# Kernel optimization log

Measured on AMD Instinct MI355X. Metric: run time of the kernel, lower is better.

Reference implementation:

```python
import jax, jax.numpy as jnp
import numpy as np

BATCH = 8192
IN_F = 1024
OUT_F = 1024
GRID_SIZE = 5
SPLINE_ORDER = 3
GRID_LO, GRID_HI = -1.0, 1.0


def setup_inputs() -> dict:
    key = jax.random.key(0)
    k1, k2, k3, k4 = jax.random.split(key, 4)
    x = jax.random.normal(k1, (BATCH, IN_F), dtype=jnp.float32)
    # grid buffer: extended knot vector, same for every input feature
    h = (GRID_HI - GRID_LO) / GRID_SIZE
    knots = jnp.linspace(GRID_LO - SPLINE_ORDER * h, GRID_HI + SPLINE_ORDER * h,
                         GRID_SIZE + 2 * SPLINE_ORDER + 1, dtype=jnp.float32)
    grid = jnp.tile(knots[None, :], (IN_F, 1))  # [in, 12]
    fan_in_scale = 1.0 / np.sqrt(IN_F)
    base_weight = jax.random.normal(k2, (OUT_F, IN_F), dtype=jnp.float32) * fan_in_scale
    spline_weight = jax.random.normal(k3, (IN_F, GRID_SIZE + SPLINE_ORDER, OUT_F), dtype=jnp.float32) * 0.1
    spline_scaler = jax.random.normal(k4, (IN_F, OUT_F), dtype=jnp.float32) * fan_in_scale
    return {"x": x, "grid": grid, "base_weight": base_weight,
            "spline_weight": spline_weight, "spline_scaler": spline_scaler}


def b_splines(x, grid):
    """Cox-de Boor recursion. x: [B, in], grid: [in, G+2k+1] -> [B, in, G+k]."""
    xe = x[:, :, None]  # [B, in, 1]
    bases = ((xe >= grid[:, :-1]) & (xe < grid[:, 1:])).astype(x.dtype)  # [B, in, G+2k]
    for k in range(1, SPLINE_ORDER + 1):
        left = (xe - grid[:, :-(k + 1)]) / (grid[:, k:-1] - grid[:, :-(k + 1)])
        right = (grid[:, k + 1:] - xe) / (grid[:, k + 1:] - grid[:, 1:-k])
        bases = left * bases[:, :, :-1] + right * bases[:, :, 1:]
    return bases  # [B, in, G+k]


def reference(x, grid, base_weight, spline_weight, spline_scaler):
    # base branch: SiLU(x) @ W_base^T
    base_out = jax.nn.silu(x) @ base_weight.T  # [B, out]
    # spline branch
    basis = b_splines(x, grid)  # [B, in, G+k]
    scaled_w = spline_weight * spline_scaler[:, None, :]  # [in, G+k, out]
    spline_out = jnp.einsum('bik,iko->bo', basis, scaled_w)  # [B, out]
    return base_out + spline_out
```

## Files before the change

kernel.cpp:

```cpp
#include <hip/hip_runtime.h>
#include <cstdint>
#include <cstddef>

#define BATCH 8192
#define IN_F 1024
#define OUT_F 1024
#define NSPL 9
#define KDIM (IN_F * NSPL)

#define BM 256
#define BN 256
#define KS (KDIM / 2)
#define NH (KS / 32)

typedef __bf16 bf16x8 __attribute__((ext_vector_type(8)));
typedef float f32x4 __attribute__((ext_vector_type(4)));

__device__ __forceinline__ void g2l16(const void* g, void* l) {
  __builtin_amdgcn_global_load_lds(
      (__attribute__((address_space(1))) void*)(g),
      (__attribute__((address_space(3))) void*)(l),
      16, 0, 0);
}

__device__ __forceinline__ void barrier_raw() {
  asm volatile("" ::: "memory");
  __builtin_amdgcn_s_barrier();
  asm volatile("" ::: "memory");
}

__global__ void build_w(const float* __restrict__ bw, const float* __restrict__ sw,
                        const float* __restrict__ sc, __bf16* __restrict__ Wt) {
  __shared__ float s_sw[16 * 8 * 64];
  __shared__ float s_sc[16 * 64];
  __shared__ float s_bw[64 * 16];
  const int tid = threadIdx.x;
  const int o0 = (blockIdx.x & 15) * 64;
  const int i0 = (blockIdx.x >> 4) * 16;

#pragma unroll
  for (int it = 0; it < 32; ++it) {
    const int t = it * 256 + tid;
    const int i = t >> 9, r = (t >> 6) & 7, oo = t & 63;
    s_sw[t] = sw[((size_t)(i0 + i) * 8 + r) * OUT_F + o0 + oo];
  }
#pragma unroll
  for (int it = 0; it < 4; ++it) {
    const int t = it * 256 + tid;
    const int i = t >> 6, oo = t & 63;
    s_sc[t] = sc[(size_t)(i0 + i) * OUT_F + o0 + oo];
  }
#pragma unroll
  for (int it = 0; it < 4; ++it) {
    const int t = it * 256 + tid;
    const int oo = t >> 4, ii = t & 15;
    s_bw[t] = bw[(size_t)(o0 + oo) * IN_F + i0 + ii];
  }
  __syncthreads();

  const int oo = tid >> 2;
  const int isub = (tid & 3) * 4;
#pragma unroll
  for (int is = 0; is < 4; ++is) {
    const int i = isub + is;
    __bf16* dst = Wt + (size_t)(o0 + oo) * KDIM + (size_t)(i0 + i) * NSPL;
    dst[0] = (__bf16)s_bw[oo * 16 + i];
    const float scal = s_sc[i * 64 + oo];
#pragma unroll
    for (int r = 0; r < 8; ++r)
      dst[1 + r] = (__bf16)(s_sw[i * 512 + r * 64 + oo] * scal);
  }
}

__global__ __launch_bounds__(256) void build_a(const float* __restrict__ x,
                                               __bf16* __restrict__ A) {
  __shared__ __align__(16) __bf16 rowbuf[2 * KDIM];
  const int tid = threadIdx.x;
  const int r2 = tid >> 7;
  const int tr = tid & 127;
  const size_t b = (size_t)blockIdx.x * 2 + r2;

  const float4* xp = (const float4*)(x + b * IN_F + (size_t)tr * 8);
  const float4 v0 = xp[0], v1 = xp[1];
  const float vv[8] = {v0.x, v0.y, v0.z, v0.w, v1.x, v1.y, v1.z, v1.w};

  union HB { __bf16 h[72]; uint4 q[9]; } hb;

#pragma unroll
  for (int f = 0; f < 8; ++f) {
    const float v = vv[f];
    const float s0 = v / (1.f + __expf(-v));
    const float p = (v + 2.2f) * 2.5f;
    const int cell = (int)floorf(p);
    const bool ok = (cell >= 0) && (cell <= 10) && (v < 2.2f);
    const float gate = ok ? (1.f / 6.f) : 0.f;
    const float t = p - (float)cell;
    const float t2 = t * t, t3 = t2 * t;
    const float omt = 1.f - t;
    const float c0 = gate * omt * omt * omt;
    const float c1 = gate * (3.f * t3 - 6.f * t2 + 4.f);
    const float c2 = gate * (-3.f * t3 + 3.f * t2 + 3.f * t + 1.f);
    const float c3 = gate * t3;
    const int j0 = cell - 3;
    hb.h[f * 9 + 0] = (__bf16)s0;
#pragma unroll
    for (int r = 0; r < 8; ++r) {
      const int d = r - j0;
      float val = (d == 0) ? c0 : 0.f;
      val = (d == 1) ? c1 : val;
      val = (d == 2) ? c2 : val;
      val = (d == 3) ? c3 : val;
      hb.h[f * 9 + 1 + r] = (__bf16)val;
    }
  }

  uint4* ldst = (uint4*)(rowbuf + (size_t)r2 * KDIM) + (size_t)tr * 9;
#pragma unroll
  for (int k = 0; k < 9; ++k) ldst[k] = hb.q[k];
  __syncthreads();

  const uint4* src = (const uint4*)rowbuf;
  uint4* dst = (uint4*)(A + (size_t)blockIdx.x * 2 * KDIM);
#pragma unroll
  for (int it = 0; it < 9; ++it)
    dst[it * 256 + tid] = src[it * 256 + tid];
}

__global__ __launch_bounds__(512, 2) void gemm_bt(const __bf16* __restrict__ A,
                                                  const __bf16* __restrict__ W,
                                                  float* __restrict__ out,
                                                  float* __restrict__ part) {
  __shared__ __align__(16) __bf16 As[4][BM * 32];
  __shared__ __align__(16) __bf16 Bs[4][BN * 32];

  const int tid = threadIdx.x;
  const int wv = tid >> 6;
  const int lane = tid & 63;

  const int bid = blockIdx.x;
  const int xcd = bid & 7;
  const int j = bid >> 3;
  const int m0 = (xcd * 4 + (j & 3)) * BM;
  const int n0 = ((j >> 2) & 3) * BN;
  const int ks = j >> 4;
  const size_t kbase = (size_t)ks * KS;

  const int wr = wv >> 2;
  const int wc = wv & 3;

  const int srow = lane >> 2;
  const int usrc = (lane & 3) ^ ((lane >> 3) & 3);
  const __bf16* gA = A + (size_t)(m0 + wv * 32 + srow) * KDIM + kbase + usrc * 8;
  const __bf16* gB = W + (size_t)(n0 + wv * 32 + srow) * KDIM + kbase + usrc * 8;

#define STAGE_HALF(s, hh)                                             \
  do {                                                                \
    const size_t ko = (size_t)(hh) * 32;                              \
    g2l16(gA + ko,                     &As[s][wv * 1024]);            \
    g2l16(gA + ko + 16 * (size_t)KDIM, &As[s][wv * 1024 + 512]);      \
    g2l16(gB + ko,                     &Bs[s][wv * 1024]);            \
    g2l16(gB + ko + 16 * (size_t)KDIM, &Bs[s][wv * 1024 + 512]);      \
  } while (0)

  const int mrow = lane & 15;
  const int quad = lane >> 4;
  const int xu = (quad ^ ((mrow >> 1) & 3)) * 8;
  int aoff[8], boff[4];
#pragma unroll
  for (int mt = 0; mt < 8; ++mt) aoff[mt] = (wr * 128 + mt * 16 + mrow) * 32 + xu;
#pragma unroll
  for (int nt = 0; nt < 4; ++nt) boff[nt] = (wc * 64 + nt * 16 + mrow) * 32 + xu;

  f32x4 acc[8][4];
  const f32x4 zero = {0.f, 0.f, 0.f, 0.f};
#pragma unroll
  for (int mt = 0; mt < 8; ++mt)
#pragma unroll
    for (int nt = 0; nt < 4; ++nt) acc[mt][nt] = zero;

  STAGE_HALF(0, 0);
  STAGE_HALF(1, 1);
  STAGE_HALF(2, 2);
  asm volatile("s_waitcnt vmcnt(8)" ::: "memory");
  barrier_raw();

  for (int h = 0; h < NH; ++h) {
    const int s = h & 3;

    bf16x8 af[8], bf[4];
#pragma unroll
    for (int mt = 0; mt < 8; ++mt) af[mt] = *(const bf16x8*)(&As[s][aoff[mt]]);
#pragma unroll
    for (int nt = 0; nt < 4; ++nt) bf[nt] = *(const bf16x8*)(&Bs[s][boff[nt]]);

    if (h + 3 < NH) {
      STAGE_HALF((h + 3) & 3, h + 3);
      asm volatile("s_waitcnt vmcnt(8)" ::: "memory");
    } else if (h + 2 < NH) {
      asm volatile("s_waitcnt vmcnt(4)" ::: "memory");
    } else {
      asm volatile("s_waitcnt vmcnt(0)" ::: "memory");
    }
    barrier_raw();

    __builtin_amdgcn_s_setprio(1);
#pragma unroll
    for (int mt = 0; mt < 8; ++mt)
#pragma unroll
      for (int nt = 0; nt < 4; ++nt)
        acc[mt][nt] = __builtin_amdgcn_mfma_f32_16x16x32_bf16(af[mt], bf[nt],
                                                              acc[mt][nt], 0, 0, 0);
    __builtin_amdgcn_s_setprio(0);
    barrier_raw();
  }

  float* __restrict__ dst = ks ? part : out;
#pragma unroll
  for (int mt = 0; mt < 8; ++mt) {
#pragma unroll
    for (int nt = 0; nt < 4; ++nt) {
      const int col = n0 + wc * 64 + nt * 16 + mrow;
      const int rbase = m0 + wr * 128 + mt * 16 + quad * 4;
#pragma unroll
      for (int r = 0; r < 4; ++r)
        dst[(size_t)(rbase + r) * OUT_F + col] = acc[mt][nt][r];
    }
  }
#undef STAGE_HALF
}

__global__ __launch_bounds__(256) void reduce_add(float* __restrict__ out,
                                                  const float* __restrict__ part) {
  const size_t base = (size_t)blockIdx.x * 256 + threadIdx.x;
  f32x4* o = (f32x4*)out;
  const f32x4* p = (const f32x4*)part;
#pragma unroll
  for (int it = 0; it < 4; ++it) {
    const size_t i = base + (size_t)it * 2048 * 256;
    f32x4 a = o[i], b = p[i];
    a.x += b.x; a.y += b.y; a.z += b.z; a.w += b.w;
    o[i] = a;
  }
}

extern "C" void kernel_launch(void* const* d_in, const int* in_sizes, int n_in,
                              void* d_out, int out_size, void* d_ws, size_t ws_size,
                              hipStream_t stream) {
  const float* x  = (const float*)d_in[0];
  const float* bw = (const float*)d_in[2];
  const float* sw = (const float*)d_in[3];
  const float* sc = (const float*)d_in[4];
  float* out = (float*)d_out;

  __bf16* Wt = (__bf16*)d_ws;
  __bf16* Ab = (__bf16*)((char*)d_ws +
                         (size_t)OUT_F * KDIM * sizeof(__bf16));
  float* part = (float*)((char*)d_ws +
                         (size_t)OUT_F * KDIM * sizeof(__bf16) +
                         (size_t)BATCH * KDIM * sizeof(__bf16));

  build_w<<<1024, 256, 0, stream>>>(bw, sw, sc, Wt);
  build_a<<<BATCH / 2, 256, 0, stream>>>(x, Ab);
  gemm_bt<<<(BATCH / BM) * (OUT_F / BN) * 2, 512, 0, stream>>>(Ab, Wt, out, part);
  reduce_add<<<2048, 256, 0, stream>>>(out, part);
}
```

Measured before the change: 291.2 us.

## Stage build_w output through LDS and split GEMM MFMA loop into two phases

build_w now writes its bf16 tile into shared memory and then stores it to global memory as coalesced 8-byte chunks, replacing the scattered 2-byte stores. In the GEMM main loop, A fragments are loaded from LDS in two halves, with extra barriers between two MFMA phases. The split is meant to interleave LDS reads with matrix ops across waves and reduce register pressure. It adds two barriers per K iteration, and the stage holding those A rows must stay valid until the second read.

```diff
diff --git a/kernel.cpp b/kernel.cpp
--- a/kernel.cpp
+++ b/kernel.cpp
@@ -29,11 +29,14 @@
   asm volatile("" ::: "memory");
 }
 
-__global__ void build_w(const float* __restrict__ bw, const float* __restrict__ sw,
-                        const float* __restrict__ sc, __bf16* __restrict__ Wt) {
+__global__ __launch_bounds__(256) void build_w(const float* __restrict__ bw,
+                                               const float* __restrict__ sw,
+                                               const float* __restrict__ sc,
+                                               __bf16* __restrict__ Wt) {
   __shared__ float s_sw[16 * 8 * 64];
   __shared__ float s_sc[16 * 64];
   __shared__ float s_bw[64 * 16];
+  __shared__ __align__(16) __bf16 s_out[64 * 144];
   const int tid = threadIdx.x;
   const int o0 = (blockIdx.x & 15) * 64;
   const int i0 = (blockIdx.x >> 4) * 16;
@@ -63,12 +66,22 @@
 #pragma unroll
   for (int is = 0; is < 4; ++is) {
     const int i = isub + is;
-    __bf16* dst = Wt + (size_t)(o0 + oo) * KDIM + (size_t)(i0 + i) * NSPL;
+    __bf16* dst = s_out + oo * 144 + i * 9;
     dst[0] = (__bf16)s_bw[oo * 16 + i];
     const float scal = s_sc[i * 64 + oo];
 #pragma unroll
     for (int r = 0; r < 8; ++r)
       dst[1 + r] = (__bf16)(s_sw[i * 512 + r * 64 + oo] * scal);
+  }
+  __syncthreads();
+
+  const uint2* s2 = (const uint2*)s_out;
+#pragma unroll
+  for (int k = 0; k < 9; ++k) {
+    const int idx = k * 256 + tid;
+    const int row = idx / 36;
+    const int col = idx - row * 36;
+    *(uint2*)(Wt + (size_t)(o0 + row) * KDIM + (size_t)i0 * 9 + col * 4) = s2[idx];
   }
 }
 
@@ -187,9 +200,9 @@
   for (int h = 0; h < NH; ++h) {
     const int s = h & 3;
 
-    bf16x8 af[8], bf[4];
-#pragma unroll
-    for (int mt = 0; mt < 8; ++mt) af[mt] = *(const bf16x8*)(&As[s][aoff[mt]]);
+    bf16x8 af[4], bf[4];
+#pragma unroll
+    for (int mt = 0; mt < 4; ++mt) af[mt] = *(const bf16x8*)(&As[s][aoff[mt]]);
 #pragma unroll
     for (int nt = 0; nt < 4; ++nt) bf[nt] = *(const bf16x8*)(&Bs[s][boff[nt]]);
 
@@ -205,11 +218,27 @@
 
     __builtin_amdgcn_s_setprio(1);
 #pragma unroll
-    for (int mt = 0; mt < 8; ++mt)
+    for (int mt = 0; mt < 4; ++mt)
 #pragma unroll
       for (int nt = 0; nt < 4; ++nt)
         acc[mt][nt] = __builtin_amdgcn_mfma_f32_16x16x32_bf16(af[mt], bf[nt],
                                                               acc[mt][nt], 0, 0, 0);
+    __builtin_amdgcn_s_setprio(0);
+    barrier_raw();
+
+    bf16x8 af2[4];
+#pragma unroll
+    for (int mt = 0; mt < 4; ++mt) af2[mt] = *(const bf16x8*)(&As[s][aoff[4 + mt]]);
+    barrier_raw();
+
+    __builtin_amdgcn_s_setprio(1);
+#pragma unroll
+    for (int mt = 0; mt < 4; ++mt)
+#pragma unroll
+      for (int nt = 0; nt < 4; ++nt)
+        acc[4 + mt][nt] = __builtin_amdgcn_mfma_f32_16x16x32_bf16(af2[mt], bf[nt],
+                                                                  acc[4 + mt][nt],
+                                                                  0, 0, 0);
     __builtin_amdgcn_s_setprio(0);
     barrier_raw();
   }
```

Measured after the change: 307.4 us. 5.6% more time.

## Compute spline basis on the fly inside GEMM instead of materializing A

Applied to the files above, without the earlier changes.

Stops writing the full expanded bf16 activation matrix (batch x 9216) to global memory. Instead the GEMM computes the B-spline bases from a transposed fp32 copy of x while staging LDS tiles; only the SiLU part is precomputed and loaded asynchronously. The weight matrix is re-laid out so that the base columns come first and the 8 spline columns per feature follow contiguously. This removes large global writes and reads for A, at the cost of extra VALU work and LDS stores inside the GEMM's main loop, which may compete with the MFMA work.

```diff
diff --git a/kernel.cpp b/kernel.cpp
--- a/kernel.cpp
+++ b/kernel.cpp
@@ -5,13 +5,12 @@
 #define BATCH 8192
 #define IN_F 1024
 #define OUT_F 1024
-#define NSPL 9
-#define KDIM (IN_F * NSPL)
+#define KDIM 9216
+#define KS 4608
+#define NH 144
 
 #define BM 256
 #define BN 256
-#define KS (KDIM / 2)
-#define NH (KS / 32)
 
 typedef __bf16 bf16x8 __attribute__((ext_vector_type(8)));
 typedef float f32x4 __attribute__((ext_vector_type(4)));
@@ -29,11 +28,38 @@
   asm volatile("" ::: "memory");
 }
 
-__global__ void build_w(const float* __restrict__ bw, const float* __restrict__ sw,
-                        const float* __restrict__ sc, __bf16* __restrict__ Wt) {
+__device__ __forceinline__ uint4 spline8(float v) {
+  const float p = (v + 2.2f) * 2.5f;
+  const int cell = (int)floorf(p);
+  const bool ok = (cell >= 0) && (cell <= 10) && (v < 2.2f);
+  const float gate = ok ? (1.f / 6.f) : 0.f;
+  const float t = p - (float)cell;
+  const float t2 = t * t, t3 = t2 * t;
+  const float omt = 1.f - t;
+  const float c0 = gate * omt * omt * omt;
+  const float c1 = gate * (3.f * t3 - 6.f * t2 + 4.f);
+  const float c2 = gate * (-3.f * t3 + 3.f * t2 + 3.f * t + 1.f);
+  const float c3 = gate * t3;
+  const int j0 = cell - 3;
+  union { __bf16 h[8]; uint4 q; } u;
+#pragma unroll
+  for (int r = 0; r < 8; ++r) {
+    const int d = r - j0;
+    float val = (d == 0) ? c0 : 0.f;
+    val = (d == 1) ? c1 : val;
+    val = (d == 2) ? c2 : val;
+    val = (d == 3) ? c3 : val;
+    u.h[r] = (__bf16)val;
+  }
+  return u.q;
+}
+
+__global__ __launch_bounds__(256) void build_w(const float* __restrict__ bw,
+                                               const float* __restrict__ sw,
+                                               const float* __restrict__ sc,
+                                               __bf16* __restrict__ Wt) {
   __shared__ float s_sw[16 * 8 * 64];
   __shared__ float s_sc[16 * 64];
-  __shared__ float s_bw[64 * 16];
   const int tid = threadIdx.x;
   const int o0 = (blockIdx.x & 15) * 64;
   const int i0 = (blockIdx.x >> 4) * 16;
@@ -50,12 +76,6 @@
     const int i = t >> 6, oo = t & 63;
     s_sc[t] = sc[(size_t)(i0 + i) * OUT_F + o0 + oo];
   }
-#pragma unroll
-  for (int it = 0; it < 4; ++it) {
-    const int t = it * 256 + tid;
-    const int oo = t >> 4, ii = t & 15;
-    s_bw[t] = bw[(size_t)(o0 + oo) * IN_F + i0 + ii];
-  }
   __syncthreads();
 
   const int oo = tid >> 2;
@@ -63,71 +83,55 @@
 #pragma unroll
   for (int is = 0; is < 4; ++is) {
     const int i = isub + is;
-    __bf16* dst = Wt + (size_t)(o0 + oo) * KDIM + (size_t)(i0 + i) * NSPL;
-    dst[0] = (__bf16)s_bw[oo * 16 + i];
     const float scal = s_sc[i * 64 + oo];
+    union { __bf16 h[8]; uint4 q; } u;
 #pragma unroll
     for (int r = 0; r < 8; ++r)
-      dst[1 + r] = (__bf16)(s_sw[i * 512 + r * 64 + oo] * scal);
-  }
-}
-
-__global__ __launch_bounds__(256) void build_a(const float* __restrict__ x,
-                                               __bf16* __restrict__ A) {
-  __shared__ __align__(16) __bf16 rowbuf[2 * KDIM];
+      u.h[r] = (__bf16)(s_sw[i * 512 + r * 64 + oo] * scal);
+    *(uint4*)(Wt + (size_t)(o0 + oo) * KDIM + 1024 + (size_t)(i0 + i) * 8) = u.q;
+  }
+
+  if ((blockIdx.x >> 4) == 0) {
+#pragma unroll
+    for (int it = 0; it < 64; ++it) {
+      const int idx = it * 256 + tid;
+      const int ooo = idx >> 8, c4 = idx & 255;
+      const float4 v = *(const float4*)(bw + (size_t)(o0 + ooo) * IN_F + c4 * 4);
+      union { __bf16 h[4]; uint2 u2; } u;
+      u.h[0] = (__bf16)v.x; u.h[1] = (__bf16)v.y;
+      u.h[2] = (__bf16)v.z; u.h[3] = (__bf16)v.w;
+      *(uint2*)(Wt + (size_t)(o0 + ooo) * KDIM + c4 * 4) = u.u2;
+    }
+  }
+}
+
+__global__ __launch_bounds__(256) void build_prep(const float* __restrict__ x,
+                                                  float* __restrict__ xT,
+                                                  __bf16* __restrict__ Asl) {
+  __shared__ float tile[64 * 65];
   const int tid = threadIdx.x;
-  const int r2 = tid >> 7;
-  const int tr = tid & 127;
-  const size_t b = (size_t)blockIdx.x * 2 + r2;
-
-  const float4* xp = (const float4*)(x + b * IN_F + (size_t)tr * 8);
-  const float4 v0 = xp[0], v1 = xp[1];
-  const float vv[8] = {v0.x, v0.y, v0.z, v0.w, v1.x, v1.y, v1.z, v1.w};
-
-  union HB { __bf16 h[72]; uint4 q[9]; } hb;
-
-#pragma unroll
-  for (int f = 0; f < 8; ++f) {
-    const float v = vv[f];
-    const float s0 = v / (1.f + __expf(-v));
-    const float p = (v + 2.2f) * 2.5f;
-    const int cell = (int)floorf(p);
-    const bool ok = (cell >= 0) && (cell <= 10) && (v < 2.2f);
-    const float gate = ok ? (1.f / 6.f) : 0.f;
-    const float t = p - (float)cell;
-    const float t2 = t * t, t3 = t2 * t;
-    const float omt = 1.f - t;
-    const float c0 = gate * omt * omt * omt;
-    const float c1 = gate * (3.f * t3 - 6.f * t2 + 4.f);
-    const float c2 = gate * (-3.f * t3 + 3.f * t2 + 3.f * t + 1.f);
-    const float c3 = gate * t3;
-    const int j0 = cell - 3;
-    hb.h[f * 9 + 0] = (__bf16)s0;
-#pragma unroll
-    for (int r = 0; r < 8; ++r) {
-      const int d = r - j0;
-      float val = (d == 0) ? c0 : 0.f;
-      val = (d == 1) ? c1 : val;
-      val = (d == 2) ? c2 : val;
-      val = (d == 3) ? c3 : val;
-      hb.h[f * 9 + 1 + r] = (__bf16)val;
-    }
-  }
-
-  uint4* ldst = (uint4*)(rowbuf + (size_t)r2 * KDIM) + (size_t)tr * 9;
-#pragma unroll
-  for (int k = 0; k < 9; ++k) ldst[k] = hb.q[k];
+  const int b0 = (blockIdx.x >> 4) * 64;
+  const int c0 = (blockIdx.x & 15) * 64;
+#pragma unroll
+  for (int it = 0; it < 16; ++it) {
+    const int idx = it * 256 + tid;
+    const int r = idx >> 6, c = idx & 63;
+    const float v = x[(size_t)(b0 + r) * IN_F + c0 + c];
+    tile[r * 65 + c] = v;
+    Asl[(size_t)(b0 + r) * IN_F + c0 + c] = (__bf16)(v / (1.f + __expf(-v)));
+  }
   __syncthreads();
-
-  const uint4* src = (const uint4*)rowbuf;
-  uint4* dst = (uint4*)(A + (size_t)blockIdx.x * 2 * KDIM);
-#pragma unroll
-  for (int it = 0; it < 9; ++it)
-    dst[it * 256 + tid] = src[it * 256 + tid];
-}
-
-__global__ __launch_bounds__(512, 2) void gemm_bt(const __bf16* __restrict__ A,
+#pragma unroll
+  for (int it = 0; it < 16; ++it) {
+    const int idx = it * 256 + tid;
+    const int f = idx >> 6, rr = idx & 63;
+    xT[(size_t)(c0 + f) * BATCH + b0 + rr] = tile[rr * 65 + f];
+  }
+}
+
+__global__ __launch_bounds__(512, 2) void gemm_bt(const __bf16* __restrict__ Asl,
                                                   const __bf16* __restrict__ W,
+                                                  const float* __restrict__ xT,
                                                   float* __restrict__ out,
                                                   float* __restrict__ part) {
   __shared__ __align__(16) __bf16 As[4][BM * 32];
@@ -150,17 +154,13 @@
 
   const int srow = lane >> 2;
   const int usrc = (lane & 3) ^ ((lane >> 3) & 3);
-  const __bf16* gA = A + (size_t)(m0 + wv * 32 + srow) * KDIM + kbase + usrc * 8;
-  const __bf16* gB = W + (size_t)(n0 + wv * 32 + srow) * KDIM + kbase + usrc * 8;
-
-#define STAGE_HALF(s, hh)                                             \
-  do {                                                                \
-    const size_t ko = (size_t)(hh) * 32;                              \
-    g2l16(gA + ko,                     &As[s][wv * 1024]);            \
-    g2l16(gA + ko + 16 * (size_t)KDIM, &As[s][wv * 1024 + 512]);      \
-    g2l16(gB + ko,                     &Bs[s][wv * 1024]);            \
-    g2l16(gB + ko + 16 * (size_t)KDIM, &Bs[s][wv * 1024 + 512]);      \
-  } while (0)
+  const __bf16* gB  = W   + (size_t)(n0 + wv * 32 + srow) * KDIM + kbase + usrc * 8;
+  const __bf16* gAs = Asl + (size_t)(m0 + wv * 32 + srow) * IN_F + usrc * 8;
+
+  const int arow_c = tid & 255;
+  const int ajc = tid >> 8;
+  const int u0x = (2 * ajc) ^ ((arow_c >> 1) & 3);
+  const int u1x = (2 * ajc + 1) ^ ((arow_c >> 1) & 3);
 
   const int mrow = lane & 15;
   const int quad = lane >> 4;
@@ -171,6 +171,30 @@
 #pragma unroll
   for (int nt = 0; nt < 4; ++nt) boff[nt] = (wc * 64 + nt * 16 + mrow) * 32 + xu;
 
+#define ISSUE(s3, t3, XN)                                                     \
+  do {                                                                        \
+    if (ks == 0 && (t3) < 32) {                                               \
+      g2l16(gAs + (size_t)(t3) * 32,              &As[s3][wv * 1024]);        \
+      g2l16(gAs + (size_t)(t3) * 32 + 16 * IN_F,  &As[s3][wv * 1024 + 512]);  \
+    } else {                                                                  \
+      const int i0_ = ks ? (448 + 4 * (t3)) : (4 * (t3) - 128);               \
+      XN.x = xT[(size_t)(i0_ + 2 * ajc) * BATCH + m0 + arow_c];               \
+      XN.y = xT[(size_t)(i0_ + 2 * ajc + 1) * BATCH + m0 + arow_c];           \
+    }                                                                         \
+    g2l16(gB + (size_t)(t3) * 32,                     &Bs[s3][wv * 1024]);    \
+    g2l16(gB + (size_t)(t3) * 32 + 16 * (size_t)KDIM, &Bs[s3][wv * 1024 + 512]); \
+  } while (0)
+
+#define COMPUTE(s2, t2, XC)                                                   \
+  do {                                                                        \
+    if (ks || (t2) >= 32) {                                                   \
+      const uint4 q0 = spline8(XC.x);                                         \
+      const uint4 q1 = spline8(XC.y);                                         \
+      *(uint4*)(&As[s2][arow_c * 32 + u0x * 8]) = q0;                         \
+      *(uint4*)(&As[s2][arow_c * 32 + u1x * 8]) = q1;                         \
+    }                                                                         \
+  } while (0)
+
   f32x4 acc[8][4];
   const f32x4 zero = {0.f, 0.f, 0.f, 0.f};
 #pragma unroll
@@ -178,40 +202,49 @@
 #pragma unroll
     for (int nt = 0; nt < 4; ++nt) acc[mt][nt] = zero;
 
-  STAGE_HALF(0, 0);
-  STAGE_HALF(1, 1);
-  STAGE_HALF(2, 2);
+  float2 xp0 = {0.f, 0.f}, xp1 = {0.f, 0.f}, xa = {0.f, 0.f}, xb = {0.f, 0.f};
+  ISSUE(0, 0, xp0);
+  ISSUE(1, 1, xp1);
+  ISSUE(2, 2, xa);
   asm volatile("s_waitcnt vmcnt(8)" ::: "memory");
+  COMPUTE(0, 0, xp0);
+  asm volatile("s_waitcnt vmcnt(4)" ::: "memory");
+  COMPUTE(1, 1, xp1);
+  asm volatile("s_waitcnt lgkmcnt(0)" ::: "memory");
   barrier_raw();
 
-  for (int h = 0; h < NH; ++h) {
-    const int s = h & 3;
-
-    bf16x8 af[8], bf[4];
-#pragma unroll
-    for (int mt = 0; mt < 8; ++mt) af[mt] = *(const bf16x8*)(&As[s][aoff[mt]]);
-#pragma unroll
-    for (int nt = 0; nt < 4; ++nt) bf[nt] = *(const bf16x8*)(&Bs[s][boff[nt]]);
-
-    if (h + 3 < NH) {
-      STAGE_HALF((h + 3) & 3, h + 3);
-      asm volatile("s_waitcnt vmcnt(8)" ::: "memory");
-    } else if (h + 2 < NH) {
-      asm volatile("s_waitcnt vmcnt(4)" ::: "memory");
-    } else {
-      asm volatile("s_waitcnt vmcnt(0)" ::: "memory");
-    }
-    barrier_raw();
-
-    __builtin_amdgcn_s_setprio(1);
-#pragma unroll
-    for (int mt = 0; mt < 8; ++mt)
-#pragma unroll
-      for (int nt = 0; nt < 4; ++nt)
-        acc[mt][nt] = __builtin_amdgcn_mfma_f32_16x16x32_bf16(af[mt], bf[nt],
-                                                              acc[mt][nt], 0, 0, 0);
-    __builtin_amdgcn_s_setprio(0);
-    barrier_raw();
+#define PHASE(h, XC, XN)                                                      \
+  do {                                                                        \
+    const int s_ = (h) & 3;                                                   \
+    bf16x8 af[8], bf[4];                                                      \
+    _Pragma("unroll")                                                         \
+    for (int mt = 0; mt < 8; ++mt) af[mt] = *(const bf16x8*)(&As[s_][aoff[mt]]); \
+    _Pragma("unroll")                                                         \
+    for (int nt = 0; nt < 4; ++nt) bf[nt] = *(const bf16x8*)(&Bs[s_][boff[nt]]); \
+    if ((h) + 3 < NH) { ISSUE(((h) + 3) & 3, (h) + 3, XN); }                  \
+    if ((h) + 2 < NH) {                                                       \
+      if ((h) + 3 < NH) { asm volatile("s_waitcnt vmcnt(4)" ::: "memory"); }  \
+      else              { asm volatile("s_waitcnt vmcnt(0)" ::: "memory"); }  \
+      COMPUTE(((h) + 2) & 3, (h) + 2, XC);                                    \
+    } else if ((h) + 1 < NH) {                                                \
+      asm volatile("s_waitcnt vmcnt(0)" ::: "memory");                        \
+    }                                                                         \
+    asm volatile("s_waitcnt lgkmcnt(0)" ::: "memory");                        \
+    barrier_raw();                                                            \
+    __builtin_amdgcn_s_setprio(1);                                            \
+    _Pragma("unroll")                                                         \
+    for (int mt = 0; mt < 8; ++mt)                                            \
+      _Pragma("unroll")                                                       \
+      for (int nt = 0; nt < 4; ++nt)                                          \
+        acc[mt][nt] = __builtin_amdgcn_mfma_f32_16x16x32_bf16(af[mt], bf[nt], \
+                                                              acc[mt][nt], 0, 0, 0); \
+    __builtin_amdgcn_s_setprio(0);                                            \
+    barrier_raw();                                                            \
+  } while (0)
+
+  for (int h = 0; h < NH; h += 2) {
+    PHASE(h, xa, xb);
+    PHASE(h + 1, xb, xa);
   }
 
   float* __restrict__ dst = ks ? part : out;
@@ -226,7 +259,9 @@
         dst[(size_t)(rbase + r) * OUT_F + col] = acc[mt][nt][r];
     }
   }
-#undef STAGE_HALF
+#undef PHASE
+#undef COMPUTE
+#undef ISSUE
 }
 
 __global__ __launch_bounds__(256) void reduce_add(float* __restrict__ out,
@@ -252,15 +287,17 @@
   const float* sc = (const float*)d_in[4];
   float* out = (float*)d_out;
 
-  __bf16* Wt = (__bf16*)d_ws;
-  __bf16* Ab = (__bf16*)((char*)d_ws +
-                         (size_t)OUT_F * KDIM * sizeof(__bf16));
-  float* part = (float*)((char*)d_ws +
-                         (size_t)OUT_F * KDIM * sizeof(__bf16) +
-                         (size_t)BATCH * KDIM * sizeof(__bf16));
+  char* ws = (char*)d_ws;
+  __bf16* Wt  = (__bf16*)ws;
+  __bf16* Asl = (__bf16*)(ws + (size_t)OUT_F * KDIM * 2);
+  float*  xT  = (float*)(ws + (size_t)OUT_F * KDIM * 2
+                            + (size_t)BATCH * IN_F * 2);
+  float* part = (float*)(ws + (size_t)OUT_F * KDIM * 2
+                            + (size_t)BATCH * IN_F * 2
+                            + (size_t)IN_F * BATCH * 4);
 
   build_w<<<1024, 256, 0, stream>>>(bw, sw, sc, Wt);
-  build_a<<<BATCH / 2, 256, 0, stream>>>(x, Ab);
-  gemm_bt<<<(BATCH / BM) * (OUT_F / BN) * 2, 512, 0, stream>>>(Ab, Wt, out, part);
+  build_prep<<<2048, 256, 0, stream>>>(x, xT, Asl);
+  gemm_bt<<<256, 512, 0, stream>>>(Asl, Wt, xT, out, part);
   reduce_add<<<2048, 256, 0, stream>>>(out, part);
 }
```

Result: slower. 399.3 us (+37.1%).

## Shrink GEMM tile to 256x128 with 4 waves and triple buffering; stage build_w output in LDS

Applied to the files above, without the earlier changes.

The GEMM block tile drops from 256x256 with 8 waves to 256x128 with 4 waves. Each wave still computes a 128x64 subtile. The LDS pipeline goes from a 4-stage ring to a 3-stage ring with a prefetch distance of two. The grid doubles so more blocks fit on each CU, at the cost of lower operand reuse per block and more total A traffic. Separately, build_w now assembles each output tile in shared memory and writes it back with coalesced 8-byte stores instead of scattered 2-byte stores.

```diff
diff --git a/kernel.cpp b/kernel.cpp
--- a/kernel.cpp
+++ b/kernel.cpp
@@ -9,7 +9,7 @@
 #define KDIM (IN_F * NSPL)
 
 #define BM 256
-#define BN 256
+#define BN 128
 #define KS (KDIM / 2)
 #define NH (KS / 32)
 
@@ -29,11 +29,14 @@
   asm volatile("" ::: "memory");
 }
 
-__global__ void build_w(const float* __restrict__ bw, const float* __restrict__ sw,
-                        const float* __restrict__ sc, __bf16* __restrict__ Wt) {
+__global__ __launch_bounds__(256) void build_w(const float* __restrict__ bw,
+                                               const float* __restrict__ sw,
+                                               const float* __restrict__ sc,
+                                               __bf16* __restrict__ Wt) {
   __shared__ float s_sw[16 * 8 * 64];
   __shared__ float s_sc[16 * 64];
   __shared__ float s_bw[64 * 16];
+  __shared__ __align__(16) __bf16 s_out[64 * 144];
   const int tid = threadIdx.x;
   const int o0 = (blockIdx.x & 15) * 64;
   const int i0 = (blockIdx.x >> 4) * 16;
@@ -63,12 +66,22 @@
 #pragma unroll
   for (int is = 0; is < 4; ++is) {
     const int i = isub + is;
-    __bf16* dst = Wt + (size_t)(o0 + oo) * KDIM + (size_t)(i0 + i) * NSPL;
+    __bf16* dst = s_out + oo * 144 + i * 9;
     dst[0] = (__bf16)s_bw[oo * 16 + i];
     const float scal = s_sc[i * 64 + oo];
 #pragma unroll
     for (int r = 0; r < 8; ++r)
       dst[1 + r] = (__bf16)(s_sw[i * 512 + r * 64 + oo] * scal);
+  }
+  __syncthreads();
+
+  const uint2* s2 = (const uint2*)s_out;
+#pragma unroll
+  for (int k = 0; k < 9; ++k) {
+    const int idx = k * 256 + tid;
+    const int row = idx / 36;
+    const int col = idx - row * 36;
+    *(uint2*)(Wt + (size_t)(o0 + row) * KDIM + (size_t)i0 * 9 + col * 4) = s2[idx];
   }
 }
 
@@ -126,12 +139,12 @@
     dst[it * 256 + tid] = src[it * 256 + tid];
 }
 
-__global__ __launch_bounds__(512, 2) void gemm_bt(const __bf16* __restrict__ A,
+__global__ __launch_bounds__(256, 2) void gemm_bt(const __bf16* __restrict__ A,
                                                   const __bf16* __restrict__ W,
                                                   float* __restrict__ out,
                                                   float* __restrict__ part) {
-  __shared__ __align__(16) __bf16 As[4][BM * 32];
-  __shared__ __align__(16) __bf16 Bs[4][BN * 32];
+  __shared__ __align__(16) __bf16 As[3][BM * 32];
+  __shared__ __align__(16) __bf16 Bs[3][BN * 32];
 
   const int tid = threadIdx.x;
   const int wv = tid >> 6;
@@ -141,25 +154,27 @@
   const int xcd = bid & 7;
   const int j = bid >> 3;
   const int m0 = (xcd * 4 + (j & 3)) * BM;
-  const int n0 = ((j >> 2) & 3) * BN;
-  const int ks = j >> 4;
+  const int n0 = ((j >> 2) & 7) * BN;
+  const int ks = j >> 5;
   const size_t kbase = (size_t)ks * KS;
 
-  const int wr = wv >> 2;
-  const int wc = wv & 3;
+  const int wr = wv >> 1;
+  const int wc = wv & 1;
 
   const int srow = lane >> 2;
   const int usrc = (lane & 3) ^ ((lane >> 3) & 3);
-  const __bf16* gA = A + (size_t)(m0 + wv * 32 + srow) * KDIM + kbase + usrc * 8;
+  const __bf16* gA = A + (size_t)(m0 + wv * 64 + srow) * KDIM + kbase + usrc * 8;
   const __bf16* gB = W + (size_t)(n0 + wv * 32 + srow) * KDIM + kbase + usrc * 8;
 
-#define STAGE_HALF(s, hh)                                             \
+#define STAGE(s, hh)                                                  \
   do {                                                                \
     const size_t ko = (size_t)(hh) * 32;                              \
-    g2l16(gA + ko,                     &As[s][wv * 1024]);            \
-    g2l16(gA + ko + 16 * (size_t)KDIM, &As[s][wv * 1024 + 512]);      \
-    g2l16(gB + ko,                     &Bs[s][wv * 1024]);            \
-    g2l16(gB + ko + 16 * (size_t)KDIM, &Bs[s][wv * 1024 + 512]);      \
+    g2l16(gA + ko,                     &As[s][(wv * 64 +  0) * 32]);  \
+    g2l16(gA + ko + 16 * (size_t)KDIM, &As[s][(wv * 64 + 16) * 32]);  \
+    g2l16(gA + ko + 32 * (size_t)KDIM, &As[s][(wv * 64 + 32) * 32]);  \
+    g2l16(gA + ko + 48 * (size_t)KDIM, &As[s][(wv * 64 + 48) * 32]);  \
+    g2l16(gB + ko,                     &Bs[s][(wv * 32 +  0) * 32]);  \
+    g2l16(gB + ko + 16 * (size_t)KDIM, &Bs[s][(wv * 32 + 16) * 32]);  \
   } while (0)
 
   const int mrow = lane & 15;
@@ -178,14 +193,14 @@
 #pragma unroll
     for (int nt = 0; nt < 4; ++nt) acc[mt][nt] = zero;
 
-  STAGE_HALF(0, 0);
-  STAGE_HALF(1, 1);
-  STAGE_HALF(2, 2);
-  asm volatile("s_waitcnt vmcnt(8)" ::: "memory");
+  STAGE(0, 0);
+  STAGE(1, 1);
+  asm volatile("s_waitcnt vmcnt(6)" ::: "memory");
   barrier_raw();
 
+  int s = 0;
   for (int h = 0; h < NH; ++h) {
-    const int s = h & 3;
+    const int sp = (s == 0) ? 2 : s - 1;
 
     bf16x8 af[8], bf[4];
 #pragma unroll
@@ -193,12 +208,10 @@
 #pragma unroll
     for (int nt = 0; nt < 4; ++nt) bf[nt] = *(const bf16x8*)(&Bs[s][boff[nt]]);
 
-    if (h + 3 < NH) {
-      STAGE_HALF((h + 3) & 3, h + 3);
-      asm volatile("s_waitcnt vmcnt(8)" ::: "memory");
-    } else if (h + 2 < NH) {
-      asm volatile("s_waitcnt vmcnt(4)" ::: "memory");
-    } else {
+    if (h + 2 < NH) {
+      STAGE(sp, h + 2);
+      asm volatile("s_waitcnt vmcnt(6)" ::: "memory");
+    } else if (h + 1 < NH) {
       asm volatile("s_waitcnt vmcnt(0)" ::: "memory");
     }
     barrier_raw();
@@ -212,6 +225,8 @@
                                                               acc[mt][nt], 0, 0, 0);
     __builtin_amdgcn_s_setprio(0);
     barrier_raw();
+
+    s = (s == 2) ? 0 : s + 1;
   }
 
   float* __restrict__ dst = ks ? part : out;
@@ -226,7 +241,7 @@
         dst[(size_t)(rbase + r) * OUT_F + col] = acc[mt][nt][r];
     }
   }
-#undef STAGE_HALF
+#undef STAGE
 }
 
 __global__ __launch_bounds__(256) void reduce_add(float* __restrict__ out,
@@ -261,6 +276,6 @@
 
   build_w<<<1024, 256, 0, stream>>>(bw, sw, sc, Wt);
   build_a<<<BATCH / 2, 256, 0, stream>>>(x, Ab);
-  gemm_bt<<<(BATCH / BM) * (OUT_F / BN) * 2, 512, 0, stream>>>(Ab, Wt, out, part);
+  gemm_bt<<<(BATCH / BM) * (OUT_F / BN) * 2, 256, 0, stream>>>(Ab, Wt, out, part);
   reduce_add<<<2048, 256, 0, stream>>>(out, part);
 }
```

Result: slower. 297.2 us (+2.1%).
